# Kernel optimization log

Hardware: AMD Instinct MI355X
Metric: run time of the kernel (lower is better)

Reference implementation:

```python
import jax, jax.numpy as jnp
import numpy as np


def setup_inputs() -> dict:
    key = jax.random.key(0)
    ks = jax.random.split(key, 7)
    B, T, H, O = 2048, 2048, 32, 2
    SCALE = 0.1  # keep gates out of deep saturation
    return {
        "x": jax.random.normal(ks[0], (B, T), dtype=jnp.float32),
        "w_ih": jax.random.normal(ks[1], (3 * H, 1), dtype=jnp.float32) * SCALE,
        "w_hh": jax.random.normal(ks[2], (3 * H, H), dtype=jnp.float32) * SCALE,
        "b_ih": jax.random.normal(ks[3], (3 * H,), dtype=jnp.float32) * SCALE,
        "b_hh": jax.random.normal(ks[4], (3 * H,), dtype=jnp.float32) * SCALE,
        "head_w": jax.random.normal(ks[5], (O, H), dtype=jnp.float32) * SCALE,
        "head_b": jax.random.normal(ks[6], (O,), dtype=jnp.float32) * SCALE,
    }


def reference(x, w_ih, w_hh, b_ih, b_hh, head_w, head_b):
    # x: [B, T] scalar time series (torch does x.unsqueeze(-1)).
    B, T = x.shape
    H = w_hh.shape[1]
    # Precompute input contributions to all 3 gates: [B, T, 3H]
    # (input_size == 1, so this is an outer product with w_ih[:, 0]).
    xg = x[:, :, None] * w_ih[:, 0] + b_ih
    xg_t = jnp.swapaxes(xg, 0, 1)  # [T, B, 3H] for scan

    def step(h, xg_step):
        gh = h @ w_hh.T + b_hh  # [B, 3H]
        xr, xz, xn = jnp.split(xg_step, 3, axis=-1)
        hr, hz, hn = jnp.split(gh, 3, axis=-1)
        r = jax.nn.sigmoid(xr + hr)
        z = jax.nn.sigmoid(xz + hz)
        n = jnp.tanh(xn + r * hn)
        h_new = (1.0 - z) * n + z * h
        return h_new, None

    h0 = jnp.zeros((B, H), dtype=x.dtype)
    hT, _ = jax.lax.scan(step, h0, xg_t)
    # head applied to last timestep's output (== final hidden state)
    return hT @ head_w.T + head_b
```

## Files before the change

### kernel.cpp

```cpp
#include <hip/hip_runtime.h>


typedef _Float16 f16x2 __attribute__((ext_vector_type(2)));

__device__ __forceinline__ float fdot2(int a, int b, float c) {
    return __builtin_amdgcn_fdot2(__builtin_bit_cast(f16x2, a),
                                  __builtin_bit_cast(f16x2, b), c, false);
}

__device__ __forceinline__ int pack_pair(float a, float b) {
    f16x2 p;
    p.x = (_Float16)a;
    p.y = (_Float16)b;
    return __builtin_bit_cast(int, p);
}

__global__ __launch_bounds__(64, 1)
void gru_scan_kernel(const float* __restrict__ x,
                     const float* __restrict__ w_ih,
                     const float* __restrict__ w_hh,
                     const float* __restrict__ b_ih,
                     const float* __restrict__ b_hh,
                     const float* __restrict__ head_w,
                     const float* __restrict__ head_b,
                     float* __restrict__ out,
                     int T)
{
    const int l = (int)threadIdx.x;
    const int g = l >> 5;
    const int j = l & 31;
    const int b = (int)blockIdx.x * 2 + g;

    __shared__ __align__(16) _Float16 h16[2][32];
    __shared__ float hf_s[2][32];
    __shared__ __align__(16) float x_s[2][2][32];

    int wR[16], wZ[16], wN[16];
    {
        const float* pR = w_hh + (     j) * 32;
        const float* pZ = w_hh + (32 + j) * 32;
        const float* pN = w_hh + (64 + j) * 32;
#pragma unroll
        for (int q = 0; q < 16; ++q) {
            wR[q] = pack_pair(pR[2*q], pR[2*q+1]);
            wZ[q] = pack_pair(pZ[2*q], pZ[2*q+1]);
            wN[q] = pack_pair(pN[2*q], pN[2*q+1]);
        }
    }

    const float wihr = w_ih[j];
    const float wihz = w_ih[32 + j];
    const float wihn = w_ih[64 + j];
    const float br   = b_ih[j]      + b_hh[j];
    const float bz   = b_ih[32 + j] + b_hh[32 + j];
    const float bni  = b_ih[64 + j];
    const float bnh  = b_hh[64 + j];

    const float* xrow   = x + (size_t)b * (size_t)T;
    const int    nchunk = T >> 5;

    float h = 0.0f;
    h16[g][j]    = (_Float16)0.0f;
    x_s[g][0][j] = xrow[j];
    float xnext  = (nchunk > 1) ? xrow[32 + j] : 0.0f;
    __builtin_amdgcn_wave_barrier();

    const int4* hq = (const int4*)(&h16[g][0]);

    for (int c = 0; c < nchunk; ++c) {
        const int buf = c & 1;
        const float* xs = &x_s[g][buf][0];
#pragma unroll 4
        for (int s = 0; s < 32; ++s) {
#pragma unroll
            for (int q = 0; q < 16; ++q) {
                asm volatile("" : "+v"(wR[q]), "+v"(wZ[q]), "+v"(wN[q]));
            }
            const float xv = xs[s];
            const int4 H0 = hq[0];
            const int4 H1 = hq[1];
            const int4 H2 = hq[2];
            const int4 H3 = hq[3];

            float rA = fdot2(H0.x, wR[ 0], fmaf(xv, wihr, br));
            float zA = fdot2(H0.x, wZ[ 0], fmaf(xv, wihz, bz));
            float nA = fdot2(H0.x, wN[ 0], bnh);
            rA = fdot2(H0.y, wR[ 1], rA); zA = fdot2(H0.y, wZ[ 1], zA); nA = fdot2(H0.y, wN[ 1], nA);
            rA = fdot2(H0.z, wR[ 2], rA); zA = fdot2(H0.z, wZ[ 2], zA); nA = fdot2(H0.z, wN[ 2], nA);
            rA = fdot2(H0.w, wR[ 3], rA); zA = fdot2(H0.w, wZ[ 3], zA); nA = fdot2(H0.w, wN[ 3], nA);

            float rB = fdot2(H1.x, wR[ 4], 0.0f);
            float zB = fdot2(H1.x, wZ[ 4], 0.0f);
            float nB = fdot2(H1.x, wN[ 4], 0.0f);
            rB = fdot2(H1.y, wR[ 5], rB); zB = fdot2(H1.y, wZ[ 5], zB); nB = fdot2(H1.y, wN[ 5], nB);
            rB = fdot2(H1.z, wR[ 6], rB); zB = fdot2(H1.z, wZ[ 6], zB); nB = fdot2(H1.z, wN[ 6], nB);
            rB = fdot2(H1.w, wR[ 7], rB); zB = fdot2(H1.w, wZ[ 7], zB); nB = fdot2(H1.w, wN[ 7], nB);

            float rC = fdot2(H2.x, wR[ 8], 0.0f);
            float zC = fdot2(H2.x, wZ[ 8], 0.0f);
            float nC = fdot2(H2.x, wN[ 8], 0.0f);
            rC = fdot2(H2.y, wR[ 9], rC); zC = fdot2(H2.y, wZ[ 9], zC); nC = fdot2(H2.y, wN[ 9], nC);
            rC = fdot2(H2.z, wR[10], rC); zC = fdot2(H2.z, wZ[10], zC); nC = fdot2(H2.z, wN[10], nC);
            rC = fdot2(H2.w, wR[11], rC); zC = fdot2(H2.w, wZ[11], zC); nC = fdot2(H2.w, wN[11], nC);

            float rD = fdot2(H3.x, wR[12], 0.0f);
            float zD = fdot2(H3.x, wZ[12], 0.0f);
            float nD = fdot2(H3.x, wN[12], 0.0f);
            rD = fdot2(H3.y, wR[13], rD); zD = fdot2(H3.y, wZ[13], zD); nD = fdot2(H3.y, wN[13], nD);
            rD = fdot2(H3.z, wR[14], rD); zD = fdot2(H3.z, wZ[14], zD); nD = fdot2(H3.z, wN[14], nD);
            rD = fdot2(H3.w, wR[15], rD); zD = fdot2(H3.w, wZ[15], zD); nD = fdot2(H3.w, wN[15], nD);

            const float rp = (rA + rB) + (rC + rD);
            const float zp = (zA + zB) + (zC + zD);
            const float np = (nA + nB) + (nC + nD);

            const float er = __builtin_amdgcn_exp2f(rp * -1.44269504088896f);
            const float ez = __builtin_amdgcn_exp2f(zp * -1.44269504088896f);
            const float A  = 1.0f + er;
            const float Bv = 1.0f + ez;
            const float inv = __builtin_amdgcn_rcpf(A * Bv);
            const float r  = Bv * inv;
            const float z  = A * inv;

            const float xn = fmaf(xv, wihn, bni);
            const float u  = fmaf(r, np, xn);
            const float et = __builtin_amdgcn_exp2f(u * 2.88539008177793f);
            const float ti = __builtin_amdgcn_rcpf(1.0f + et);
            const float n  = fmaf(-2.0f, ti, 1.0f);

            h = fmaf(z, h - n, n);
            __builtin_amdgcn_wave_barrier();
            h16[g][j] = (_Float16)h;
            __builtin_amdgcn_wave_barrier();
        }
        if (c + 1 < nchunk) {
            x_s[g][1 - buf][j] = xnext;
            if (c + 2 < nchunk) xnext = xrow[(c + 2) * 32 + j];
            __builtin_amdgcn_wave_barrier();
        }
    }

    hf_s[g][j] = h;
    __builtin_amdgcn_wave_barrier();
    if (l < 4) {
        const int g2 = l >> 1, o = l & 1;
        float acc = head_b[o];
        const float* hw = head_w + o * 32;
#pragma unroll
        for (int k = 0; k < 32; ++k) acc = fmaf(hf_s[g2][k], hw[k], acc);
        out[((int)blockIdx.x * 2 + g2) * 2 + o] = acc;
    }
}

extern "C" void kernel_launch(void* const* d_in, const int* in_sizes, int n_in,
                              void* d_out, int out_size, void* d_ws, size_t ws_size,
                              hipStream_t stream) {
    const float* x      = (const float*)d_in[0];
    const float* w_ih   = (const float*)d_in[1];
    const float* w_hh   = (const float*)d_in[2];
    const float* b_ih   = (const float*)d_in[3];
    const float* b_hh   = (const float*)d_in[4];
    const float* head_w = (const float*)d_in[5];
    const float* head_b = (const float*)d_in[6];
    float* out = (float*)d_out;

    const int B = out_size / 2;
    const int T = in_sizes[0] / B;

    dim3 grid(B / 2), block(64);
    hipLaunchKernelGGL(gru_scan_kernel, grid, block, 0, stream,
                       x, w_ih, w_hh, b_ih, b_hh, head_w, head_b, out, T);
}
```

Baseline: 487.0 us.

## Broadcast hidden state via DPP and ds_bpermute instead of LDS round-trip

Replaces the per-step shared-memory store and four 128-bit loads of the fp16 hidden vector. Each lane now packs its half value with its neighbour's via a DPP swap and v_perm, then gathers the 16 packed pairs with ds_bpermute into registers. It also hoists the asm register-pinning out of the inner loop and computes the r and z sigmoids with separate reciprocals instead of the shared-reciprocal trick. The 16 bpermutes still go through the LDS crossbar, and they may add more instructions and latency than the 4 vector loads they replace.

```diff
diff --git a/kernel.cpp b/kernel.cpp
--- a/kernel.cpp
+++ b/kernel.cpp
@@ -31,7 +31,6 @@
     const int j = l & 31;
     const int b = (int)blockIdx.x * 2 + g;
 
-    __shared__ __align__(16) _Float16 h16[2][32];
     __shared__ float hf_s[2][32];
     __shared__ __align__(16) float x_s[2][2][32];
 
@@ -47,6 +46,10 @@
             wN[q] = pack_pair(pN[2*q], pN[2*q+1]);
         }
     }
+#pragma unroll
+    for (int q = 0; q < 16; ++q) {
+        asm volatile("" : "+v"(wR[q]), "+v"(wZ[q]), "+v"(wN[q]));
+    }
 
     const float wihr = w_ih[j];
     const float wihz = w_ih[32 + j];
@@ -56,71 +59,63 @@
     const float bni  = b_ih[64 + j];
     const float bnh  = b_hh[64 + j];
 
+    const unsigned int psel = (j & 1) ? 0x05040100u : 0x01000504u;
+    const int bbase = g * 128;
+
     const float* xrow   = x + (size_t)b * (size_t)T;
     const int    nchunk = T >> 5;
 
     float h = 0.0f;
-    h16[g][j]    = (_Float16)0.0f;
+    int P0=0,P1=0,P2=0,P3=0,P4=0,P5=0,P6=0,P7=0;
+    int P8=0,P9=0,P10=0,P11=0,P12=0,P13=0,P14=0,P15=0;
+
     x_s[g][0][j] = xrow[j];
     float xnext  = (nchunk > 1) ? xrow[32 + j] : 0.0f;
     __builtin_amdgcn_wave_barrier();
-
-    const int4* hq = (const int4*)(&h16[g][0]);
 
     for (int c = 0; c < nchunk; ++c) {
         const int buf = c & 1;
         const float* xs = &x_s[g][buf][0];
 #pragma unroll 4
         for (int s = 0; s < 32; ++s) {
-#pragma unroll
-            for (int q = 0; q < 16; ++q) {
-                asm volatile("" : "+v"(wR[q]), "+v"(wZ[q]), "+v"(wN[q]));
-            }
             const float xv = xs[s];
-            const int4 H0 = hq[0];
-            const int4 H1 = hq[1];
-            const int4 H2 = hq[2];
-            const int4 H3 = hq[3];
 
-            float rA = fdot2(H0.x, wR[ 0], fmaf(xv, wihr, br));
-            float zA = fdot2(H0.x, wZ[ 0], fmaf(xv, wihz, bz));
-            float nA = fdot2(H0.x, wN[ 0], bnh);
-            rA = fdot2(H0.y, wR[ 1], rA); zA = fdot2(H0.y, wZ[ 1], zA); nA = fdot2(H0.y, wN[ 1], nA);
-            rA = fdot2(H0.z, wR[ 2], rA); zA = fdot2(H0.z, wZ[ 2], zA); nA = fdot2(H0.z, wN[ 2], nA);
-            rA = fdot2(H0.w, wR[ 3], rA); zA = fdot2(H0.w, wZ[ 3], zA); nA = fdot2(H0.w, wN[ 3], nA);
+            float rA = fdot2(P0, wR[ 0], fmaf(xv, wihr, br));
+            float zA = fdot2(P0, wZ[ 0], fmaf(xv, wihz, bz));
+            float nA = fdot2(P0, wN[ 0], bnh);
+            rA = fdot2(P1, wR[ 1], rA); zA = fdot2(P1, wZ[ 1], zA); nA = fdot2(P1, wN[ 1], nA);
+            rA = fdot2(P2, wR[ 2], rA); zA = fdot2(P2, wZ[ 2], zA); nA = fdot2(P2, wN[ 2], nA);
+            rA = fdot2(P3, wR[ 3], rA); zA = fdot2(P3, wZ[ 3], zA); nA = fdot2(P3, wN[ 3], nA);
 
-            float rB = fdot2(H1.x, wR[ 4], 0.0f);
-            float zB = fdot2(H1.x, wZ[ 4], 0.0f);
-            float nB = fdot2(H1.x, wN[ 4], 0.0f);
-            rB = fdot2(H1.y, wR[ 5], rB); zB = fdot2(H1.y, wZ[ 5], zB); nB = fdot2(H1.y, wN[ 5], nB);
-            rB = fdot2(H1.z, wR[ 6], rB); zB = fdot2(H1.z, wZ[ 6], zB); nB = fdot2(H1.z, wN[ 6], nB);
-            rB = fdot2(H1.w, wR[ 7], rB); zB = fdot2(H1.w, wZ[ 7], zB); nB = fdot2(H1.w, wN[ 7], nB);
+            float rB = fdot2(P4, wR[ 4], 0.0f);
+            float zB = fdot2(P4, wZ[ 4], 0.0f);
+            float nB = fdot2(P4, wN[ 4], 0.0f);
+            rB = fdot2(P5, wR[ 5], rB); zB = fdot2(P5, wZ[ 5], zB); nB = fdot2(P5, wN[ 5], nB);
+            rB = fdot2(P6, wR[ 6], rB); zB = fdot2(P6, wZ[ 6], zB); nB = fdot2(P6, wN[ 6], nB);
+            rB = fdot2(P7, wR[ 7], rB); zB = fdot2(P7, wZ[ 7], zB); nB = fdot2(P7, wN[ 7], nB);
 
-            float rC = fdot2(H2.x, wR[ 8], 0.0f);
-            float zC = fdot2(H2.x, wZ[ 8], 0.0f);
-            float nC = fdot2(H2.x, wN[ 8], 0.0f);
-            rC = fdot2(H2.y, wR[ 9], rC); zC = fdot2(H2.y, wZ[ 9], zC); nC = fdot2(H2.y, wN[ 9], nC);
-            rC = fdot2(H2.z, wR[10], rC); zC = fdot2(H2.z, wZ[10], zC); nC = fdot2(H2.z, wN[10], nC);
-            rC = fdot2(H2.w, wR[11], rC); zC = fdot2(H2.w, wZ[11], zC); nC = fdot2(H2.w, wN[11], nC);
+            float rC = fdot2(P8, wR[ 8], 0.0f);
+            float zC = fdot2(P8, wZ[ 8], 0.0f);
+            float nC = fdot2(P8, wN[ 8], 0.0f);
+            rC = fdot2(P9,  wR[ 9], rC); zC = fdot2(P9,  wZ[ 9], zC); nC = fdot2(P9,  wN[ 9], nC);
+            rC = fdot2(P10, wR[10], rC); zC = fdot2(P10, wZ[10], zC); nC = fdot2(P10, wN[10], nC);
+            rC = fdot2(P11, wR[11], rC); zC = fdot2(P11, wZ[11], zC); nC = fdot2(P11, wN[11], nC);
 
-            float rD = fdot2(H3.x, wR[12], 0.0f);
-            float zD = fdot2(H3.x, wZ[12], 0.0f);
-            float nD = fdot2(H3.x, wN[12], 0.0f);
-            rD = fdot2(H3.y, wR[13], rD); zD = fdot2(H3.y, wZ[13], zD); nD = fdot2(H3.y, wN[13], nD);
-            rD = fdot2(H3.z, wR[14], rD); zD = fdot2(H3.z, wZ[14], zD); nD = fdot2(H3.z, wN[14], nD);
-            rD = fdot2(H3.w, wR[15], rD); zD = fdot2(H3.w, wZ[15], zD); nD = fdot2(H3.w, wN[15], nD);
+            float rD = fdot2(P12, wR[12], 0.0f);
+            float zD = fdot2(P12, wZ[12], 0.0f);
+            float nD = fdot2(P12, wN[12], 0.0f);
+            rD = fdot2(P13, wR[13], rD); zD = fdot2(P13, wZ[13], zD); nD = fdot2(P13, wN[13], nD);
+            rD = fdot2(P14, wR[14], rD); zD = fdot2(P14, wZ[14], zD); nD = fdot2(P14, wN[14], nD);
+            rD = fdot2(P15, wR[15], rD); zD = fdot2(P15, wZ[15], zD); nD = fdot2(P15, wN[15], nD);
 
             const float rp = (rA + rB) + (rC + rD);
             const float zp = (zA + zB) + (zC + zD);
             const float np = (nA + nB) + (nC + nD);
 
             const float er = __builtin_amdgcn_exp2f(rp * -1.44269504088896f);
+            const float r  = __builtin_amdgcn_rcpf(1.0f + er);
             const float ez = __builtin_amdgcn_exp2f(zp * -1.44269504088896f);
-            const float A  = 1.0f + er;
-            const float Bv = 1.0f + ez;
-            const float inv = __builtin_amdgcn_rcpf(A * Bv);
-            const float r  = Bv * inv;
-            const float z  = A * inv;
+            const float z  = __builtin_amdgcn_rcpf(1.0f + ez);
 
             const float xn = fmaf(xv, wihn, bni);
             const float u  = fmaf(r, np, xn);
@@ -129,9 +124,29 @@
             const float n  = fmaf(-2.0f, ti, 1.0f);
 
             h = fmaf(z, h - n, n);
-            __builtin_amdgcn_wave_barrier();
-            h16[g][j] = (_Float16)h;
-            __builtin_amdgcn_wave_barrier();
+
+            const int own = (int)(unsigned int)
+                __builtin_bit_cast(unsigned short, (_Float16)h);
+            const int oth = __builtin_amdgcn_update_dpp(own, own, 0xB1,
+                                                        0xF, 0xF, true);
+            const int pk = (int)__builtin_amdgcn_perm(
+                (unsigned int)own, (unsigned int)oth, psel);
+            P0  = __builtin_amdgcn_ds_bpermute(bbase +   0, pk);
+            P1  = __builtin_amdgcn_ds_bpermute(bbase +   8, pk);
+            P2  = __builtin_amdgcn_ds_bpermute(bbase +  16, pk);
+            P3  = __builtin_amdgcn_ds_bpermute(bbase +  24, pk);
+            P4  = __builtin_amdgcn_ds_bpermute(bbase +  32, pk);
+            P5  = __builtin_amdgcn_ds_bpermute(bbase +  40, pk);
+            P6  = __builtin_amdgcn_ds_bpermute(bbase +  48, pk);
+            P7  = __builtin_amdgcn_ds_bpermute(bbase +  56, pk);
+            P8  = __builtin_amdgcn_ds_bpermute(bbase +  64, pk);
+            P9  = __builtin_amdgcn_ds_bpermute(bbase +  72, pk);
+            P10 = __builtin_amdgcn_ds_bpermute(bbase +  80, pk);
+            P11 = __builtin_amdgcn_ds_bpermute(bbase +  88, pk);
+            P12 = __builtin_amdgcn_ds_bpermute(bbase +  96, pk);
+            P13 = __builtin_amdgcn_ds_bpermute(bbase + 104, pk);
+            P14 = __builtin_amdgcn_ds_bpermute(bbase + 112, pk);
+            P15 = __builtin_amdgcn_ds_bpermute(bbase + 120, pk);
         }
         if (c + 1 < nchunk) {
             x_s[g][1 - buf][j] = xnext;
```

After: 644.0 us. +32.2%, slower.

## Stream x via per-lane float4 register prefetch and use separate sigmoid reciprocals

Applied to the files above, without the earlier changes.

Drops the shared-memory double buffer for x. Each lane now loads the same float4 of its row from global memory and keeps a two-deep register prefetch, so the per-step LDS read of x and the per-chunk staging store go away. The weight-pinning asm barrier moves out of the step loop to run once after setup. The shared-reciprocal sigmoid trick is replaced by two independent rcp calls, which shortens the dependency chain but adds one transcendental per step. All 32 lanes issue redundant broadcast global loads, and latency hiding now depends on the prefetch distance.

```diff
diff --git a/kernel.cpp b/kernel.cpp
--- a/kernel.cpp
+++ b/kernel.cpp
@@ -33,7 +33,6 @@
 
     __shared__ __align__(16) _Float16 h16[2][32];
     __shared__ float hf_s[2][32];
-    __shared__ __align__(16) float x_s[2][2][32];
 
     int wR[16], wZ[16], wN[16];
     {
@@ -47,6 +46,10 @@
             wN[q] = pack_pair(pN[2*q], pN[2*q+1]);
         }
     }
+#pragma unroll
+    for (int q = 0; q < 16; ++q) {
+        asm volatile("" : "+v"(wR[q]), "+v"(wZ[q]), "+v"(wN[q]));
+    }
 
     const float wihr = w_ih[j];
     const float wihz = w_ih[32 + j];
@@ -56,27 +59,29 @@
     const float bni  = b_ih[64 + j];
     const float bnh  = b_hh[64 + j];
 
-    const float* xrow   = x + (size_t)b * (size_t)T;
-    const int    nchunk = T >> 5;
+    const float*  xrow  = x + (size_t)b * (size_t)T;
+    const float4* xrow4 = (const float4*)xrow;
+    const int     n4    = T >> 2;
+    const int     t4max = n4 - 1;
 
     float h = 0.0f;
-    h16[g][j]    = (_Float16)0.0f;
-    x_s[g][0][j] = xrow[j];
-    float xnext  = (nchunk > 1) ? xrow[32 + j] : 0.0f;
+    h16[g][j] = (_Float16)0.0f;
     __builtin_amdgcn_wave_barrier();
 
     const int4* hq = (const int4*)(&h16[g][0]);
 
-    for (int c = 0; c < nchunk; ++c) {
-        const int buf = c & 1;
-        const float* xs = &x_s[g][buf][0];
-#pragma unroll 4
-        for (int s = 0; s < 32; ++s) {
+    float4 xcur = xrow4[0];
+    float4 xnxt = xrow4[1 <= t4max ? 1 : 0];
+
+    for (int t4 = 0; t4 < n4; ++t4) {
+        const float4 xg = xcur;
+        xcur = xnxt;
+        const int nidx = (t4 + 2 <= t4max) ? (t4 + 2) : t4max;
+        xnxt = xrow4[nidx];
 #pragma unroll
-            for (int q = 0; q < 16; ++q) {
-                asm volatile("" : "+v"(wR[q]), "+v"(wZ[q]), "+v"(wN[q]));
-            }
-            const float xv = xs[s];
+        for (int s = 0; s < 4; ++s) {
+            const float xv = (s == 0) ? xg.x : (s == 1) ? xg.y
+                           : (s == 2) ? xg.z : xg.w;
             const int4 H0 = hq[0];
             const int4 H1 = hq[1];
             const int4 H2 = hq[2];
@@ -115,12 +120,9 @@
             const float np = (nA + nB) + (nC + nD);
 
             const float er = __builtin_amdgcn_exp2f(rp * -1.44269504088896f);
+            const float r  = __builtin_amdgcn_rcpf(1.0f + er);
             const float ez = __builtin_amdgcn_exp2f(zp * -1.44269504088896f);
-            const float A  = 1.0f + er;
-            const float Bv = 1.0f + ez;
-            const float inv = __builtin_amdgcn_rcpf(A * Bv);
-            const float r  = Bv * inv;
-            const float z  = A * inv;
+            const float z  = __builtin_amdgcn_rcpf(1.0f + ez);
 
             const float xn = fmaf(xv, wihn, bni);
             const float u  = fmaf(r, np, xn);
@@ -131,11 +133,6 @@
             h = fmaf(z, h - n, n);
             __builtin_amdgcn_wave_barrier();
             h16[g][j] = (_Float16)h;
-            __builtin_amdgcn_wave_barrier();
-        }
-        if (c + 1 < nchunk) {
-            x_s[g][1 - buf][j] = xnext;
-            if (c + 2 < nchunk) xnext = xrow[(c + 2) * 32 + j];
             __builtin_amdgcn_wave_barrier();
         }
     }
```

New measurement: 508.9 us. 1.04x slower.
